# Optimization experiments

Measured on AMD Instinct MI355X. Metric: run time of the kernel, lower is better.

Reference implementation:

```python
import jax, jax.numpy as jnp
import numpy as np

N = 3072        # nodes
F_IN = 512      # input_dim
F_OUT = 256     # output_dim
ORDER = 2       # Cayley polynomial order
JACOBI = 3      # Jacobi fixed-point iterations per order


def setup_inputs() -> dict:
    key = jax.random.key(0)
    k1, k2, k3, k4, k5 = jax.random.split(key, 5)
    # normalized-adjacency-like matrix: row sums ~1 so h*Laplacian is well scaled
    adj = jax.random.uniform(k1, (N, N), dtype=jnp.float32) * (2.0 / N)
    x = jax.random.normal(k2, (N, F_IN), dtype=jnp.float32)
    h = jnp.float32(1.0)  # spectral zoom parameter
    w0 = jax.random.normal(k3, (F_IN, F_OUT), dtype=jnp.float32) * 0.05
    wr = jax.random.normal(k4, (ORDER, F_IN, F_OUT), dtype=jnp.float32) * 0.05
    wi = jax.random.normal(k5, (ORDER, F_IN, F_OUT), dtype=jnp.float32) * 0.05
    return {"x": x, "adj": adj, "h": h, "w0": w0, "wr": wr, "wi": wi}


def _cayley_forward(x, adj, h, w0, wr, wi):
    c64 = jnp.complex64
    j1 = jnp.asarray(1j, dtype=c64)
    n = adj.shape[0]
    I = jnp.eye(n, dtype=jnp.float32)
    # h * Laplacian, L = I - A_norm  (complex64, as in the TF code)
    hL = (h * (I - adj)).astype(c64)
    # Jacobi diagonal: rowsum(hL) + i  (constant across iterations)
    diag_inv = 1.0 / (jnp.sum(hL, axis=1) + j1)  # [n]

    # support[0] = I  ->  real part of I @ (x @ w0) is just x @ w0
    out = x @ w0  # [n, F_OUT] float32

    xc = x.astype(c64)
    csum = jnp.zeros((n, w0.shape[1]), dtype=c64)
    prev = I.astype(c64)
    for j in range(ORDER):
        # rhs of the linear system: x_j = hL @ prev - i*prev
        xj = hL @ prev - j1 * prev
        # Jacobi iterations: y <- y + D^{-1} (x_j - (hL @ y + i*y))
        y = xj
        for _ in range(JACOBI):
            y = y + diag_inv[:, None] * (xj - (hL @ y + j1 * y))
        W = jax.lax.complex(wr[j], wi[j])          # [F_IN, F_OUT] complex64
        csum = csum + y @ (xc @ W)                  # support_j @ pre_sup
        prev = y
    out = out + 2.0 * jnp.real(csum).astype(jnp.float32)
    return jax.nn.relu(out)


def reference(x, adj, h, w0, wr, wi):
    return _cayley_forward(x, adj, h, w0, wr, wi)
```

## Files before the change

kernel.cpp:

```cpp
#include <hip/hip_runtime.h>
#include <hip/hip_bf16.h>

#define NN 3072
#define FIN 512
#define FOUT 256

typedef __attribute__((ext_vector_type(8))) short short8;
typedef __attribute__((ext_vector_type(4))) float f32x4;

__device__ __forceinline__ short f2bf(float f) {
  union { float f; unsigned u; } v; v.f = f;
  unsigned r = v.u + 0x7fffu + ((v.u >> 16) & 1u);
  return (short)(r >> 16);
}

__device__ __forceinline__ void glds16(const short* g, short* l) {
  __builtin_amdgcn_global_load_lds(
      (const __attribute__((address_space(1))) unsigned*)g,
      (__attribute__((address_space(3))) unsigned*)l, 16, 0, 0);
}

template<int N> __device__ __forceinline__ void wait_vm() {
  if constexpr (N == 0)      asm volatile("s_waitcnt vmcnt(0)" ::: "memory");
  else if constexpr (N == 6) asm volatile("s_waitcnt vmcnt(6)" ::: "memory");
  else                       asm volatile("s_waitcnt vmcnt(8)" ::: "memory");
}


__global__ __launch_bounds__(256) void prep_adj(const float* __restrict__ adj,
    short* __restrict__ adjbf, float2* __restrict__ dinv, const float* __restrict__ hptr)
{
  int m = blockIdx.x;
  int tid = threadIdx.x;
  const float4* row = (const float4*)(adj + (size_t)m * NN);
  short4* obf = (short4*)(adjbf + (size_t)m * NN);
  float sum = 0.f;
#pragma unroll
  for (int i = 0; i < NN / 4 / 256; ++i) {
    int idx = i * 256 + tid;
    float4 v = row[idx];
    sum += (v.x + v.y) + (v.z + v.w);
    obf[idx] = make_short4(f2bf(v.x), f2bf(v.y), f2bf(v.z), f2bf(v.w));
  }
#pragma unroll
  for (int off = 32; off > 0; off >>= 1) sum += __shfl_down(sum, off, 64);
  __shared__ float red[4];
  if ((tid & 63) == 0) red[tid >> 6] = sum;
  __syncthreads();
  if (tid == 0) {
    float s = red[0] + red[1] + red[2] + red[3];
    float h = hptr[0];
    float r = h * (1.f - s);
    float den = r * r + 1.f;
    dinv[m] = make_float2(r / den, -1.f / den);
  }
}

__global__ __launch_bounds__(256) void prep_x(const float* __restrict__ x, short* __restrict__ xbf) {
  int idx = blockIdx.x * 256 + threadIdx.x;
  float4 v = ((const float4*)x)[idx];
  ((short4*)xbf)[idx] = make_short4(f2bf(v.x), f2bf(v.y), f2bf(v.z), f2bf(v.w));
}

__global__ __launch_bounds__(256) void prep_w(const float* __restrict__ w0,
    const float* __restrict__ wr, const float* __restrict__ wi, short* __restrict__ wpack)
{
  int idx = blockIdx.x * 256 + threadIdx.x;
  int f = idx & 511;
  int i = idx >> 9;
  float v;
  if (i < 1024) {
    int j = (i < 512) ? 1 : 0;
    int local = i & 511;
    int c = local >> 1;
    const float* src = (local & 1) ? wi : wr;
    v = src[((size_t)j * FIN + f) * FOUT + c];
  } else {
    v = w0[(size_t)f * FOUT + (i - 1024)];
  }
  wpack[idx] = f2bf(v);
}

template<int BM, int MR, int MODE, int KTOT>
__global__ __launch_bounds__(512, 2) void gemm_k(
    const short* __restrict__ Apan, int lda,
    const short* __restrict__ Badj, int ldb,
    const float* __restrict__ Vin,
    const float* __restrict__ Yin,
    float* __restrict__ Fout,
    short* __restrict__ Bout,
    const float2* __restrict__ dinv,
    const float* __restrict__ hptr)
{
  constexpr int BK = 64;
  constexpr int NT = KTOT / (2 * BK);
  constexpr int ALOADS = BM / 8;
  constexpr int BLOADS = 16;
  constexpr int LPW = (ALOADS + BLOADS) / 4;

  __shared__ short As[2][2][BM * BK];
  __shared__ short Bs[2][2][128 * BK];

  const int tid  = threadIdx.x;
  const int lane = tid & 63;
  const int w    = tid >> 6;
  const int g    = w >> 2;
  const int wg   = w & 3;
  const int wrow = wg >> 1, wcol = wg & 1;
  const int l15  = lane & 15;

  const int i0 = blockIdx.y * BM;
  const int j0 = blockIdx.x * 128;
  const int kbase = g * (KTOT / 2);

  const int srow = lane >> 3;
  const int scol = ((lane & 7) ^ srow) * 8;

  const short* aSrc = Apan + (size_t)i0 * lda + kbase;
  const short* bSrc = Badj + (size_t)j0 * ldb + kbase;

  auto STAGE = [&](int t) {
    const int k0 = t * BK;
    short* at = As[g][t & 1];
    short* bt = Bs[g][t & 1];
#pragma unroll
    for (int li = 0; li < ALOADS / 4; ++li) {
      int rb = (wg + li * 4) * 8;
      glds16(aSrc + (size_t)(rb + srow) * lda + k0 + scol, at + rb * BK);
    }
#pragma unroll
    for (int li = 0; li < BLOADS / 4; ++li) {
      int rb = (wg + li * 4) * 8;
      glds16(bSrc + (size_t)(rb + srow) * ldb + k0 + scol, bt + rb * BK);
    }
  };

  f32x4 acc[MR][4];
#pragma unroll
  for (int a = 0; a < MR; a++)
#pragma unroll
    for (int b = 0; b < 4; b++) acc[a][b] = (f32x4){0.f, 0.f, 0.f, 0.f};

  STAGE(0);
  STAGE(1);

  for (int t = 0; t < NT; ++t) {
    if (t < NT - 1) wait_vm<LPW>(); else wait_vm<0>();
    __builtin_amdgcn_s_barrier();
    asm volatile("" ::: "memory");

    const short* at = As[g][t & 1];
    const short* bt = Bs[g][t & 1];
#pragma unroll
    for (int kk = 0; kk < 2; ++kk) {
      const int cbase = kk * 4 + (lane >> 4);
      short8 af[MR], bfg[4];
#pragma unroll
      for (int a = 0; a < MR; ++a) {
        int ra = wrow * (MR * 16) + a * 16 + l15;
        int c = cbase ^ (ra & 7);
        af[a] = *(const short8*)(at + ra * BK + c * 8);
      }
#pragma unroll
      for (int b = 0; b < 4; ++b) {
        int rb = wcol * 64 + b * 16 + l15;
        int c = cbase ^ (rb & 7);
        bfg[b] = *(const short8*)(bt + rb * BK + c * 8);
      }
      __builtin_amdgcn_s_setprio(1);
#pragma unroll
      for (int a = 0; a < MR; ++a)
#pragma unroll
        for (int b = 0; b < 4; ++b)
          acc[a][b] = __builtin_amdgcn_mfma_f32_16x16x32_bf16(af[a], bfg[b], acc[a][b], 0, 0, 0);
      __builtin_amdgcn_s_setprio(0);
    }

    asm volatile("" ::: "memory");
    __builtin_amdgcn_s_barrier();
    asm volatile("" ::: "memory");
    if (t + 2 < NT) STAGE(t + 2);
  }

  float* red = (float*)&As[0][0][0];
  const int rl0 = wrow * (MR * 16) + ((lane >> 4) << 2);
  const int cl0 = wcol * 64 + l15;
  if (g == 1) {
#pragma unroll
    for (int a = 0; a < MR; ++a)
#pragma unroll
      for (int b = 0; b < 4; ++b)
#pragma unroll
        for (int q = 0; q < 4; ++q)
          red[(size_t)(rl0 + a * 16 + q) * 128 + cl0 + b * 16] = acc[a][b][q];
  }
  __syncthreads();

  if (g == 0) {
    const float hv = hptr[0];
#pragma unroll
    for (int a = 0; a < MR; ++a) {
#pragma unroll
      for (int b = 0; b < 4; ++b) {
        f32x4 c = acc[a][b];
        const int rl = rl0 + a * 16;
        const int cl = cl0 + b * 16;
#pragma unroll
        for (int q = 0; q < 4; ++q)
          c[q] += red[(size_t)(rl + q) * 128 + cl];
        const int ia = i0 + rl;
        const int jb = j0 + cl;
        if (MODE == 0) {
#pragma unroll
          for (int q = 0; q < 4; ++q) {
            size_t off = (size_t)(ia + q) * NN + jb;
            Fout[off] = c[q];
            if (ia + q < 1024) Bout[off] = f2bf(c[q]);
          }
        } else if (MODE == 1) {
#pragma unroll
          for (int p = 0; p < 4; p += 2) {
            size_t offr = (size_t)(ia + p) * NN + jb;
            size_t offi = offr + NN;
            float vr = Vin[offr], vi = Vin[offi];
            float outr = hv * (vr - c[p])     + vi;
            float outi = hv * (vi - c[p + 1]) - vr;
            Fout[offr] = outr; Fout[offi] = outi;
            Bout[offr] = f2bf(outr); Bout[offi] = f2bf(outi);
          }
        } else {
#pragma unroll
          for (int p = 0; p < 4; p += 2) {
            size_t offr = (size_t)(ia + p) * NN + jb;
            size_t offi = offr + NN;
            float2 dv = dinv[jb];
            float vr = Vin[offr], vi = Vin[offi];
            float yr = Yin[offr], yi = Yin[offi];
            float tr_ = hv * (yr - c[p])     - yi;
            float ti_ = hv * (yi - c[p + 1]) + yr;
            float er = vr - tr_, ei = vi - ti_;
            float nyr = yr + dv.x * er - dv.y * ei;
            float nyi = yi + dv.x * ei + dv.y * er;
            Fout[offr] = nyr; Fout[offi] = nyi;
            Bout[offr] = f2bf(nyr); Bout[offi] = f2bf(nyi);
          }
        }
      }
    }
  }
}

__global__ __launch_bounds__(256) void final_out(
    const float* __restrict__ Vbuf,
    const float* __restrict__ ybuf,
    float* __restrict__ out)
{
  __shared__ float t[64][65];
  int n0 = blockIdx.x * 64;
  int c0 = blockIdx.y * 64;
  int lane = threadIdx.x & 63;
  int wv = threadIdx.x >> 6;
#pragma unroll
  for (int s = 0; s < 16; s++) {
    int c = c0 + wv + s * 4;
    float o0 = Vbuf[(size_t)(1024 + c) * NN + n0 + lane];
    float u  = ybuf[(size_t)(2 * c) * NN + n0 + lane];
    float sv = ybuf[(size_t)(512 + 2 * c) * NN + n0 + lane];
    float v = o0 + 2.f * (u + sv);
    t[lane][wv + s * 4] = v > 0.f ? v : 0.f;
  }
  __syncthreads();
#pragma unroll
  for (int s = 0; s < 16; s++) {
    int nl = wv + s * 4;
    out[(size_t)(n0 + nl) * FOUT + c0 + lane] = t[nl][lane];
  }
}

extern "C" void kernel_launch(void* const* d_in, const int* in_sizes, int n_in,
                              void* d_out, int out_size, void* d_ws, size_t ws_size,
                              hipStream_t stream) {
  const float* x   = (const float*)d_in[0];
  const float* adj = (const float*)d_in[1];
  const float* h   = (const float*)d_in[2];
  const float* w0  = (const float*)d_in[3];
  const float* wr  = (const float*)d_in[4];
  const float* wi  = (const float*)d_in[5];
  float* out = (float*)d_out;

  char* ws = (char*)d_ws;
  size_t off = 0;
  auto alloc = [&](size_t bytes) {
    char* p = ws + off;
    off += (bytes + 255) & ~(size_t)255;
    return p;
  };
  short*  adjbf = (short*)alloc((size_t)NN * NN * 2);
  short*  xbf   = (short*)alloc((size_t)NN * FIN * 2);
  short*  wpack = (short*)alloc((size_t)1280 * FIN * 2);
  float2* dinv  = (float2*)alloc((size_t)NN * sizeof(float2));
  float*  Vbuf  = (float*)alloc((size_t)1280 * NN * 4);
  float*  ybuf  = (float*)alloc((size_t)1024 * NN * 4);
  short*  b0    = (short*)alloc((size_t)1024 * NN * 2);
  short*  b1    = (short*)alloc((size_t)1024 * NN * 2);

  prep_adj<<<NN, 256, 0, stream>>>(adj, adjbf, dinv, h);
  prep_x<<<(NN * FIN / 4) / 256, 256, 0, stream>>>(x, xbf);
  prep_w<<<(1280 * FIN) / 256, 256, 0, stream>>>(w0, wr, wi, wpack);

  gemm_k<128, 4, 0, FIN><<<dim3(24, 10), 512, 0, stream>>>(
      wpack, FIN, xbf, FIN, nullptr, nullptr, Vbuf, b0, dinv, h);
  gemm_k<128, 4, 1, NN><<<dim3(24, 8), 512, 0, stream>>>(
      b0, NN, adjbf, NN, Vbuf, nullptr, Vbuf, b1, dinv, h);
  gemm_k<128, 4, 2, NN><<<dim3(24, 8), 512, 0, stream>>>(
      b1, NN, adjbf, NN, Vbuf, Vbuf, ybuf, b0, dinv, h);
  gemm_k<128, 4, 2, NN><<<dim3(24, 8), 512, 0, stream>>>(
      b0, NN, adjbf, NN, Vbuf, ybuf, ybuf, b1, dinv, h);
  gemm_k<128, 4, 2, NN><<<dim3(24, 8), 512, 0, stream>>>(
      b1, NN, adjbf, NN, Vbuf, ybuf, ybuf, b0, dinv, h);
  gemm_k<64, 2, 1, NN><<<dim3(24, 8), 512, 0, stream>>>(
      b0, NN, adjbf, NN, ybuf, nullptr, Vbuf, b1, dinv, h);
  gemm_k<64, 2, 2, NN><<<dim3(24, 8), 512, 0, stream>>>(
      b1, NN, adjbf, NN, Vbuf, Vbuf, ybuf, b0, dinv, h);
  gemm_k<64, 2, 2, NN><<<dim3(24, 8), 512, 0, stream>>>(
      b0, NN, adjbf, NN, Vbuf, ybuf, ybuf, b1, dinv, h);
  gemm_k<64, 2, 2, NN><<<dim3(24, 8), 512, 0, stream>>>(
      b1, NN, adjbf, NN, Vbuf, ybuf, ybuf, b0, dinv, h);

  final_out<<<dim3(48, 4), 256, 0, stream>>>(Vbuf, ybuf, out);
}
```

Baseline: 387.6 us.

## Replace intra-block split-K GEMM with cross-block split-K and atomic tile reduction

The two-group in-block K split with double-buffered LDS is replaced by a single-group 256-thread kernel. It splits K across up to 4 blocks, each writing fp32 partials to a workspace slab. The last block to arrive, detected with a per-tile atomic counter, reduces the partials and runs the fused epilogue. Block indices are remapped so column tiles group by XCD. This raises the number of blocks per GEMM to fill the CUs, but drops double buffering, adds fp32 partial traffic and needs a counter memset.

```diff
diff --git a/kernel.cpp b/kernel.cpp
--- a/kernel.cpp
+++ b/kernel.cpp
@@ -18,12 +18,6 @@
   __builtin_amdgcn_global_load_lds(
       (const __attribute__((address_space(1))) unsigned*)g,
       (__attribute__((address_space(3))) unsigned*)l, 16, 0, 0);
-}
-
-template<int N> __device__ __forceinline__ void wait_vm() {
-  if constexpr (N == 0)      asm volatile("s_waitcnt vmcnt(0)" ::: "memory");
-  else if constexpr (N == 6) asm volatile("s_waitcnt vmcnt(6)" ::: "memory");
-  else                       asm volatile("s_waitcnt vmcnt(8)" ::: "memory");
 }
 
 
@@ -81,37 +75,44 @@
   wpack[idx] = f2bf(v);
 }
 
-template<int BM, int MR, int MODE, int KTOT>
-__global__ __launch_bounds__(512, 2) void gemm_k(
+__global__ __launch_bounds__(256, 4) void gemm_sk(
     const short* __restrict__ Apan, int lda,
     const short* __restrict__ Badj, int ldb,
+    int rows, int sk, int kper, int mode,
     const float* __restrict__ Vin,
     const float* __restrict__ Yin,
     float* __restrict__ Fout,
     short* __restrict__ Bout,
+    float* __restrict__ partial,
+    int* __restrict__ cnt,
     const float2* __restrict__ dinv,
     const float* __restrict__ hptr)
 {
   constexpr int BK = 64;
-  constexpr int NT = KTOT / (2 * BK);
-  constexpr int ALOADS = BM / 8;
-  constexpr int BLOADS = 16;
-  constexpr int LPW = (ALOADS + BLOADS) / 4;
-
-  __shared__ short As[2][2][BM * BK];
-  __shared__ short Bs[2][2][128 * BK];
+  const size_t SLAB = (size_t)1280 * NN;
+
+  __shared__ short As[128 * BK];
+  __shared__ short Bs[128 * BK];
+  __shared__ int s_ord;
 
   const int tid  = threadIdx.x;
   const int lane = tid & 63;
   const int w    = tid >> 6;
-  const int g    = w >> 2;
-  const int wg   = w & 3;
-  const int wrow = wg >> 1, wcol = wg & 1;
   const int l15  = lane & 15;
 
-  const int i0 = blockIdx.y * BM;
-  const int j0 = blockIdx.x * 128;
-  const int kbase = g * (KTOT / 2);
+  const int f    = blockIdx.x;
+  const int xcd  = f & 7;
+  const int s    = f >> 3;
+  const int perj = rows * sk;
+  const int j    = xcd * 3 + s / perj;
+  const int rr   = s % perj;
+  const int i    = rr % rows;
+  const int z    = rr / rows;
+
+  const int i0 = i * 128;
+  const int j0 = j * 128;
+  const int kbase = z * kper;
+  const int NT = kper / BK;
 
   const int srow = lane >> 3;
   const int scol = ((lane & 7) ^ srow) * 8;
@@ -121,129 +122,125 @@
 
   auto STAGE = [&](int t) {
     const int k0 = t * BK;
-    short* at = As[g][t & 1];
-    short* bt = Bs[g][t & 1];
-#pragma unroll
-    for (int li = 0; li < ALOADS / 4; ++li) {
-      int rb = (wg + li * 4) * 8;
-      glds16(aSrc + (size_t)(rb + srow) * lda + k0 + scol, at + rb * BK);
-    }
-#pragma unroll
-    for (int li = 0; li < BLOADS / 4; ++li) {
-      int rb = (wg + li * 4) * 8;
-      glds16(bSrc + (size_t)(rb + srow) * ldb + k0 + scol, bt + rb * BK);
+#pragma unroll
+    for (int li = 0; li < 4; ++li) {
+      int rb = (w + li * 4) * 8;
+      glds16(aSrc + (size_t)(rb + srow) * lda + k0 + scol, As + rb * BK);
+      glds16(bSrc + (size_t)(rb + srow) * ldb + k0 + scol, Bs + rb * BK);
     }
   };
 
-  f32x4 acc[MR][4];
-#pragma unroll
-  for (int a = 0; a < MR; a++)
+  f32x4 acc[4][4];
+#pragma unroll
+  for (int a = 0; a < 4; a++)
 #pragma unroll
     for (int b = 0; b < 4; b++) acc[a][b] = (f32x4){0.f, 0.f, 0.f, 0.f};
 
+  const int wrow = w >> 1, wcol = w & 1;
+
   STAGE(0);
-  STAGE(1);
-
   for (int t = 0; t < NT; ++t) {
-    if (t < NT - 1) wait_vm<LPW>(); else wait_vm<0>();
-    __builtin_amdgcn_s_barrier();
-    asm volatile("" ::: "memory");
-
-    const short* at = As[g][t & 1];
-    const short* bt = Bs[g][t & 1];
+    __syncthreads();
 #pragma unroll
     for (int kk = 0; kk < 2; ++kk) {
-      const int cbase = kk * 4 + (lane >> 4);
-      short8 af[MR], bfg[4];
-#pragma unroll
-      for (int a = 0; a < MR; ++a) {
-        int ra = wrow * (MR * 16) + a * 16 + l15;
-        int c = cbase ^ (ra & 7);
-        af[a] = *(const short8*)(at + ra * BK + c * 8);
+      const int cb = kk * 4 + (lane >> 4);
+      short8 af[4], bfr[4];
+#pragma unroll
+      for (int a = 0; a < 4; ++a) {
+        int ra = wrow * 64 + a * 16 + l15;
+        int c = cb ^ (ra & 7);
+        af[a] = *(const short8*)(As + ra * BK + c * 8);
       }
 #pragma unroll
       for (int b = 0; b < 4; ++b) {
         int rb = wcol * 64 + b * 16 + l15;
-        int c = cbase ^ (rb & 7);
-        bfg[b] = *(const short8*)(bt + rb * BK + c * 8);
-      }
-      __builtin_amdgcn_s_setprio(1);
-#pragma unroll
-      for (int a = 0; a < MR; ++a)
+        int c = cb ^ (rb & 7);
+        bfr[b] = *(const short8*)(Bs + rb * BK + c * 8);
+      }
+#pragma unroll
+      for (int a = 0; a < 4; ++a)
 #pragma unroll
         for (int b = 0; b < 4; ++b)
-          acc[a][b] = __builtin_amdgcn_mfma_f32_16x16x32_bf16(af[a], bfg[b], acc[a][b], 0, 0, 0);
-      __builtin_amdgcn_s_setprio(0);
+          acc[a][b] = __builtin_amdgcn_mfma_f32_16x16x32_bf16(af[a], bfr[b], acc[a][b], 0, 0, 0);
     }
-
-    asm volatile("" ::: "memory");
-    __builtin_amdgcn_s_barrier();
-    asm volatile("" ::: "memory");
-    if (t + 2 < NT) STAGE(t + 2);
-  }
-
-  float* red = (float*)&As[0][0][0];
-  const int rl0 = wrow * (MR * 16) + ((lane >> 4) << 2);
-  const int cl0 = wcol * 64 + l15;
-  if (g == 1) {
-#pragma unroll
-    for (int a = 0; a < MR; ++a)
-#pragma unroll
-      for (int b = 0; b < 4; ++b)
+    __syncthreads();
+    if (t + 1 < NT) STAGE(t + 1);
+  }
+
+  const int ib = i0 + wrow * 64 + ((lane >> 4) << 2);
+  const int tile = j * rows + i;
+
+  if (sk > 1) {
+    float* ps = partial + (size_t)z * SLAB;
+#pragma unroll
+    for (int a = 0; a < 4; ++a) {
+      int ia = ib + a * 16;
+#pragma unroll
+      for (int b = 0; b < 4; ++b) {
+        int jb = j0 + wcol * 64 + b * 16 + l15;
 #pragma unroll
         for (int q = 0; q < 4; ++q)
-          red[(size_t)(rl0 + a * 16 + q) * 128 + cl0 + b * 16] = acc[a][b][q];
-  }
-  __syncthreads();
-
-  if (g == 0) {
-    const float hv = hptr[0];
-#pragma unroll
-    for (int a = 0; a < MR; ++a) {
-#pragma unroll
-      for (int b = 0; b < 4; ++b) {
-        f32x4 c = acc[a][b];
-        const int rl = rl0 + a * 16;
-        const int cl = cl0 + b * 16;
-#pragma unroll
-        for (int q = 0; q < 4; ++q)
-          c[q] += red[(size_t)(rl + q) * 128 + cl];
-        const int ia = i0 + rl;
-        const int jb = j0 + cl;
-        if (MODE == 0) {
-#pragma unroll
-          for (int q = 0; q < 4; ++q) {
-            size_t off = (size_t)(ia + q) * NN + jb;
-            Fout[off] = c[q];
-            if (ia + q < 1024) Bout[off] = f2bf(c[q]);
-          }
-        } else if (MODE == 1) {
-#pragma unroll
-          for (int p = 0; p < 4; p += 2) {
-            size_t offr = (size_t)(ia + p) * NN + jb;
-            size_t offi = offr + NN;
-            float vr = Vin[offr], vi = Vin[offi];
-            float outr = hv * (vr - c[p])     + vi;
-            float outi = hv * (vi - c[p + 1]) - vr;
-            Fout[offr] = outr; Fout[offi] = outi;
-            Bout[offr] = f2bf(outr); Bout[offi] = f2bf(outi);
-          }
-        } else {
-#pragma unroll
-          for (int p = 0; p < 4; p += 2) {
-            size_t offr = (size_t)(ia + p) * NN + jb;
-            size_t offi = offr + NN;
-            float2 dv = dinv[jb];
-            float vr = Vin[offr], vi = Vin[offi];
-            float yr = Yin[offr], yi = Yin[offi];
-            float tr_ = hv * (yr - c[p])     - yi;
-            float ti_ = hv * (yi - c[p + 1]) + yr;
-            float er = vr - tr_, ei = vi - ti_;
-            float nyr = yr + dv.x * er - dv.y * ei;
-            float nyi = yi + dv.x * ei + dv.y * er;
-            Fout[offr] = nyr; Fout[offi] = nyi;
-            Bout[offr] = f2bf(nyr); Bout[offi] = f2bf(nyi);
-          }
+          ps[(size_t)(ia + q) * NN + jb] = acc[a][b][q];
+      }
+    }
+    __threadfence();
+    __syncthreads();
+    if (tid == 0) s_ord = atomicAdd(&cnt[tile], 1);
+    __syncthreads();
+    if (s_ord != sk - 1) return;
+    __threadfence();
+  }
+
+  const float hv = hptr[0];
+#pragma unroll
+  for (int a = 0; a < 4; ++a) {
+    int ia = ib + a * 16;
+#pragma unroll
+    for (int b = 0; b < 4; ++b) {
+      int jb = j0 + wcol * 64 + b * 16 + l15;
+      f32x4 c = acc[a][b];
+      if (sk > 1) {
+        for (int z2 = 0; z2 < sk; ++z2) {
+          if (z2 == z) continue;
+          const float* ps = partial + (size_t)z2 * SLAB;
+#pragma unroll
+          for (int q = 0; q < 4; ++q)
+            c[q] += ps[(size_t)(ia + q) * NN + jb];
+        }
+      }
+      if (mode == 0) {
+#pragma unroll
+        for (int q = 0; q < 4; ++q) {
+          size_t off = (size_t)(ia + q) * NN + jb;
+          Fout[off] = c[q];
+          if (ia + q < 1024) Bout[off] = f2bf(c[q]);
+        }
+      } else if (mode == 1) {
+#pragma unroll
+        for (int p = 0; p < 4; p += 2) {
+          size_t offr = (size_t)(ia + p) * NN + jb;
+          size_t offi = offr + NN;
+          float vr = Vin[offr], vi = Vin[offi];
+          float outr = hv * (vr - c[p])     + vi;
+          float outi = hv * (vi - c[p + 1]) - vr;
+          Fout[offr] = outr; Fout[offi] = outi;
+          Bout[offr] = f2bf(outr); Bout[offi] = f2bf(outi);
+        }
+      } else {
+#pragma unroll
+        for (int p = 0; p < 4; p += 2) {
+          size_t offr = (size_t)(ia + p) * NN + jb;
+          size_t offi = offr + NN;
+          float2 dv = dinv[jb];
+          float vr = Vin[offr], vi = Vin[offi];
+          float yr = Yin[offr], yi = Yin[offi];
+          float tr_ = hv * (yr - c[p])     - yi;
+          float ti_ = hv * (yi - c[p + 1]) + yr;
+          float er = vr - tr_, ei = vi - ti_;
+          float nyr = yr + dv.x * er - dv.y * ei;
+          float nyi = yi + dv.x * ei + dv.y * er;
+          Fout[offr] = nyr; Fout[offi] = nyi;
+          Bout[offr] = f2bf(nyr); Bout[offi] = f2bf(nyi);
         }
       }
     }
@@ -304,28 +301,37 @@
   short*  b0    = (short*)alloc((size_t)1024 * NN * 2);
   short*  b1    = (short*)alloc((size_t)1024 * NN * 2);
 
+  size_t slab = (size_t)1280 * NN * 4;
+  size_t cntB = 9 * 256 * sizeof(int);
+  int sk = 1;
+  if (ws_size >= off + 4 * slab + cntB + 4096) sk = 4;
+  else if (ws_size >= off + 2 * slab + cntB + 4096) sk = 2;
+  float* partial = (float*)alloc((size_t)sk * slab);
+  int*   cnt     = (int*)alloc(cntB);
+  int sk0 = (sk >= 2) ? 2 : 1;
+
+  hipMemsetAsync(cnt, 0, cntB, stream);
   prep_adj<<<NN, 256, 0, stream>>>(adj, adjbf, dinv, h);
   prep_x<<<(NN * FIN / 4) / 256, 256, 0, stream>>>(x, xbf);
   prep_w<<<(1280 * FIN) / 256, 256, 0, stream>>>(w0, wr, wi, wpack);
 
-  gemm_k<128, 4, 0, FIN><<<dim3(24, 10), 512, 0, stream>>>(
-      wpack, FIN, xbf, FIN, nullptr, nullptr, Vbuf, b0, dinv, h);
-  gemm_k<128, 4, 1, NN><<<dim3(24, 8), 512, 0, stream>>>(
-      b0, NN, adjbf, NN, Vbuf, nullptr, Vbuf, b1, dinv, h);
-  gemm_k<128, 4, 2, NN><<<dim3(24, 8), 512, 0, stream>>>(
-      b1, NN, adjbf, NN, Vbuf, Vbuf, ybuf, b0, dinv, h);
-  gemm_k<128, 4, 2, NN><<<dim3(24, 8), 512, 0, stream>>>(
-      b0, NN, adjbf, NN, Vbuf, ybuf, ybuf, b1, dinv, h);
-  gemm_k<128, 4, 2, NN><<<dim3(24, 8), 512, 0, stream>>>(
-      b1, NN, adjbf, NN, Vbuf, ybuf, ybuf, b0, dinv, h);
-  gemm_k<64, 2, 1, NN><<<dim3(24, 8), 512, 0, stream>>>(
-      b0, NN, adjbf, NN, ybuf, nullptr, Vbuf, b1, dinv, h);
-  gemm_k<64, 2, 2, NN><<<dim3(24, 8), 512, 0, stream>>>(
-      b1, NN, adjbf, NN, Vbuf, Vbuf, ybuf, b0, dinv, h);
-  gemm_k<64, 2, 2, NN><<<dim3(24, 8), 512, 0, stream>>>(
-      b0, NN, adjbf, NN, Vbuf, ybuf, ybuf, b1, dinv, h);
-  gemm_k<64, 2, 2, NN><<<dim3(24, 8), 512, 0, stream>>>(
-      b1, NN, adjbf, NN, Vbuf, ybuf, ybuf, b0, dinv, h);
+  auto G = [&](int rows, int skv, int kper, int mode,
+               const short* A, int lda, const short* B, int ldb,
+               const float* Vin, const float* Yin, float* Fout, short* Bout, int didx) {
+    gemm_sk<<<dim3(24 * rows * skv), 256, 0, stream>>>(
+        A, lda, B, ldb, rows, skv, kper, mode,
+        Vin, Yin, Fout, Bout, partial, cnt + didx * 256, dinv, h);
+  };
+
+  G(10, sk0, FIN / sk0, 0, wpack, FIN, xbf, FIN, nullptr, nullptr, Vbuf, b0, 0);
+  G(8, sk, NN / sk, 1, b0, NN, adjbf, NN, Vbuf, nullptr, Vbuf, b1, 1);
+  G(8, sk, NN / sk, 2, b1, NN, adjbf, NN, Vbuf, Vbuf, ybuf, b0, 2);
+  G(8, sk, NN / sk, 2, b0, NN, adjbf, NN, Vbuf, ybuf, ybuf, b1, 3);
+  G(8, sk, NN / sk, 2, b1, NN, adjbf, NN, Vbuf, ybuf, ybuf, b0, 4);
+  G(4, sk, NN / sk, 1, b0, NN, adjbf, NN, ybuf, nullptr, Vbuf, b1, 5);
+  G(4, sk, NN / sk, 2, b1, NN, adjbf, NN, Vbuf, Vbuf, ybuf, b0, 6);
+  G(4, sk, NN / sk, 2, b0, NN, adjbf, NN, Vbuf, ybuf, ybuf, b1, 7);
+  G(4, sk, NN / sk, 2, b1, NN, adjbf, NN, Vbuf, ybuf, ybuf, b0, 8);
 
   final_out<<<dim3(48, 4), 256, 0, stream>>>(Vbuf, ybuf, out);
 }
```

After: 1.375 ms. 255% more time.

## Replace split-K 512-thread GEMM with 64x96 tiles and no reduction

Applied to the files above, without the earlier changes.

Replaces the split-K GEMM, where two 4-wave groups each handled half of K and were reduced through LDS, with a single 4-wave block that runs the full K loop over a 64x96 output tile. The grid grows from 24x8 to 32x16 (or 32x8) blocks, so more CUs get work on the 256-CU part and the LDS reduction and extra sync go away. In exchange each block does twice as many K iterations, has smaller MFMA tiles with less operand reuse, and drops the setprio hints.

```diff
diff --git a/kernel.cpp b/kernel.cpp
--- a/kernel.cpp
+++ b/kernel.cpp
@@ -22,8 +22,8 @@
 
 template<int N> __device__ __forceinline__ void wait_vm() {
   if constexpr (N == 0)      asm volatile("s_waitcnt vmcnt(0)" ::: "memory");
-  else if constexpr (N == 6) asm volatile("s_waitcnt vmcnt(6)" ::: "memory");
-  else                       asm volatile("s_waitcnt vmcnt(8)" ::: "memory");
+  else if constexpr (N == 5) asm volatile("s_waitcnt vmcnt(5)" ::: "memory");
+  else                       asm volatile("s_waitcnt vmcnt(10)" ::: "memory");
 }
 
 
@@ -81,8 +81,8 @@
   wpack[idx] = f2bf(v);
 }
 
-template<int BM, int MR, int MODE, int KTOT>
-__global__ __launch_bounds__(512, 2) void gemm_k(
+template<int MODE, int KTOT>
+__global__ __launch_bounds__(256, 2) void gemm_t(
     const short* __restrict__ Apan, int lda,
     const short* __restrict__ Badj, int ldb,
     const float* __restrict__ Vin,
@@ -93,53 +93,53 @@
     const float* __restrict__ hptr)
 {
   constexpr int BK = 64;
-  constexpr int NT = KTOT / (2 * BK);
-  constexpr int ALOADS = BM / 8;
-  constexpr int BLOADS = 16;
-  constexpr int LPW = (ALOADS + BLOADS) / 4;
-
-  __shared__ short As[2][2][BM * BK];
-  __shared__ short Bs[2][2][128 * BK];
+  constexpr int BM = 64;
+  constexpr int BN = 96;
+  constexpr int NT = KTOT / BK;
+  constexpr int MR = 2;
+  constexpr int AL = 2;
+  constexpr int BL = 3;
+  constexpr int LPW = AL + BL;
+
+  __shared__ short As[2][BM * BK];
+  __shared__ short Bs[2][BN * BK];
 
   const int tid  = threadIdx.x;
   const int lane = tid & 63;
   const int w    = tid >> 6;
-  const int g    = w >> 2;
-  const int wg   = w & 3;
-  const int wrow = wg >> 1, wcol = wg & 1;
   const int l15  = lane & 15;
+  const int wrow = w >> 1, wcol = w & 1;
 
   const int i0 = blockIdx.y * BM;
-  const int j0 = blockIdx.x * 128;
-  const int kbase = g * (KTOT / 2);
+  const int j0 = blockIdx.x * BN;
 
   const int srow = lane >> 3;
   const int scol = ((lane & 7) ^ srow) * 8;
 
-  const short* aSrc = Apan + (size_t)i0 * lda + kbase;
-  const short* bSrc = Badj + (size_t)j0 * ldb + kbase;
+  const short* aSrc = Apan + (size_t)i0 * lda;
+  const short* bSrc = Badj + (size_t)j0 * ldb;
 
   auto STAGE = [&](int t) {
     const int k0 = t * BK;
-    short* at = As[g][t & 1];
-    short* bt = Bs[g][t & 1];
-#pragma unroll
-    for (int li = 0; li < ALOADS / 4; ++li) {
-      int rb = (wg + li * 4) * 8;
+    short* at = As[t & 1];
+    short* bt = Bs[t & 1];
+#pragma unroll
+    for (int li = 0; li < AL; ++li) {
+      int rb = (w + li * 4) * 8;
       glds16(aSrc + (size_t)(rb + srow) * lda + k0 + scol, at + rb * BK);
     }
 #pragma unroll
-    for (int li = 0; li < BLOADS / 4; ++li) {
-      int rb = (wg + li * 4) * 8;
+    for (int li = 0; li < BL; ++li) {
+      int rb = (w + li * 4) * 8;
       glds16(bSrc + (size_t)(rb + srow) * ldb + k0 + scol, bt + rb * BK);
     }
   };
 
-  f32x4 acc[MR][4];
+  f32x4 acc[MR][3];
 #pragma unroll
   for (int a = 0; a < MR; a++)
 #pragma unroll
-    for (int b = 0; b < 4; b++) acc[a][b] = (f32x4){0.f, 0.f, 0.f, 0.f};
+    for (int b = 0; b < 3; b++) acc[a][b] = (f32x4){0.f, 0.f, 0.f, 0.f};
 
   STAGE(0);
   STAGE(1);
@@ -149,31 +149,29 @@
     __builtin_amdgcn_s_barrier();
     asm volatile("" ::: "memory");
 
-    const short* at = As[g][t & 1];
-    const short* bt = Bs[g][t & 1];
+    const short* at = As[t & 1];
+    const short* bt = Bs[t & 1];
 #pragma unroll
     for (int kk = 0; kk < 2; ++kk) {
-      const int cbase = kk * 4 + (lane >> 4);
-      short8 af[MR], bfg[4];
+      const int cb = kk * 4 + (lane >> 4);
+      short8 af[MR], bfr[3];
 #pragma unroll
       for (int a = 0; a < MR; ++a) {
-        int ra = wrow * (MR * 16) + a * 16 + l15;
-        int c = cbase ^ (ra & 7);
+        int ra = wrow * 32 + a * 16 + l15;
+        int c = cb ^ (ra & 7);
         af[a] = *(const short8*)(at + ra * BK + c * 8);
       }
 #pragma unroll
-      for (int b = 0; b < 4; ++b) {
-        int rb = wcol * 64 + b * 16 + l15;
-        int c = cbase ^ (rb & 7);
-        bfg[b] = *(const short8*)(bt + rb * BK + c * 8);
+      for (int b = 0; b < 3; ++b) {
+        int rb = wcol * 48 + b * 16 + l15;
+        int c = cb ^ (rb & 7);
+        bfr[b] = *(const short8*)(bt + rb * BK + c * 8);
       }
-      __builtin_amdgcn_s_setprio(1);
 #pragma unroll
       for (int a = 0; a < MR; ++a)
 #pragma unroll
-        for (int b = 0; b < 4; ++b)
-          acc[a][b] = __builtin_amdgcn_mfma_f32_16x16x32_bf16(af[a], bfg[b], acc[a][b], 0, 0, 0);
-      __builtin_amdgcn_s_setprio(0);
+        for (int b = 0; b < 3; ++b)
+          acc[a][b] = __builtin_amdgcn_mfma_f32_16x16x32_bf16(af[a], bfr[b], acc[a][b], 0, 0, 0);
     }
 
     asm volatile("" ::: "memory");
@@ -182,68 +180,48 @@
     if (t + 2 < NT) STAGE(t + 2);
   }
 
-  float* red = (float*)&As[0][0][0];
-  const int rl0 = wrow * (MR * 16) + ((lane >> 4) << 2);
-  const int cl0 = wcol * 64 + l15;
-  if (g == 1) {
-#pragma unroll
-    for (int a = 0; a < MR; ++a)
-#pragma unroll
-      for (int b = 0; b < 4; ++b)
-#pragma unroll
-        for (int q = 0; q < 4; ++q)
-          red[(size_t)(rl0 + a * 16 + q) * 128 + cl0 + b * 16] = acc[a][b][q];
-  }
-  __syncthreads();
-
-  if (g == 0) {
-    const float hv = hptr[0];
-#pragma unroll
-    for (int a = 0; a < MR; ++a) {
-#pragma unroll
-      for (int b = 0; b < 4; ++b) {
-        f32x4 c = acc[a][b];
-        const int rl = rl0 + a * 16;
-        const int cl = cl0 + b * 16;
-#pragma unroll
-        for (int q = 0; q < 4; ++q)
-          c[q] += red[(size_t)(rl + q) * 128 + cl];
-        const int ia = i0 + rl;
-        const int jb = j0 + cl;
-        if (MODE == 0) {
-#pragma unroll
-          for (int q = 0; q < 4; ++q) {
-            size_t off = (size_t)(ia + q) * NN + jb;
-            Fout[off] = c[q];
-            if (ia + q < 1024) Bout[off] = f2bf(c[q]);
-          }
-        } else if (MODE == 1) {
-#pragma unroll
-          for (int p = 0; p < 4; p += 2) {
-            size_t offr = (size_t)(ia + p) * NN + jb;
-            size_t offi = offr + NN;
-            float vr = Vin[offr], vi = Vin[offi];
-            float outr = hv * (vr - c[p])     + vi;
-            float outi = hv * (vi - c[p + 1]) - vr;
-            Fout[offr] = outr; Fout[offi] = outi;
-            Bout[offr] = f2bf(outr); Bout[offi] = f2bf(outi);
-          }
-        } else {
-#pragma unroll
-          for (int p = 0; p < 4; p += 2) {
-            size_t offr = (size_t)(ia + p) * NN + jb;
-            size_t offi = offr + NN;
-            float2 dv = dinv[jb];
-            float vr = Vin[offr], vi = Vin[offi];
-            float yr = Yin[offr], yi = Yin[offi];
-            float tr_ = hv * (yr - c[p])     - yi;
-            float ti_ = hv * (yi - c[p + 1]) + yr;
-            float er = vr - tr_, ei = vi - ti_;
-            float nyr = yr + dv.x * er - dv.y * ei;
-            float nyi = yi + dv.x * ei + dv.y * er;
-            Fout[offr] = nyr; Fout[offi] = nyi;
-            Bout[offr] = f2bf(nyr); Bout[offi] = f2bf(nyi);
-          }
+  const float hv = hptr[0];
+  const int ibase = i0 + wrow * 32 + ((lane >> 4) << 2);
+#pragma unroll
+  for (int a = 0; a < MR; ++a) {
+    const int ia = ibase + a * 16;
+#pragma unroll
+    for (int b = 0; b < 3; ++b) {
+      const int jb = j0 + wcol * 48 + b * 16 + l15;
+      f32x4 c = acc[a][b];
+      if (MODE == 0) {
+#pragma unroll
+        for (int q = 0; q < 4; ++q) {
+          size_t off = (size_t)(ia + q) * NN + jb;
+          Fout[off] = c[q];
+          if (ia + q < 1024) Bout[off] = f2bf(c[q]);
+        }
+      } else if (MODE == 1) {
+#pragma unroll
+        for (int p = 0; p < 4; p += 2) {
+          size_t offr = (size_t)(ia + p) * NN + jb;
+          size_t offi = offr + NN;
+          float vr = Vin[offr], vi = Vin[offi];
+          float outr = hv * (vr - c[p])     + vi;
+          float outi = hv * (vi - c[p + 1]) - vr;
+          Fout[offr] = outr; Fout[offi] = outi;
+          Bout[offr] = f2bf(outr); Bout[offi] = f2bf(outi);
+        }
+      } else {
+#pragma unroll
+        for (int p = 0; p < 4; p += 2) {
+          size_t offr = (size_t)(ia + p) * NN + jb;
+          size_t offi = offr + NN;
+          float2 dv = dinv[jb];
+          float vr = Vin[offr], vi = Vin[offi];
+          float yr = Yin[offr], yi = Yin[offi];
+          float tr_ = hv * (yr - c[p])     - yi;
+          float ti_ = hv * (yi - c[p + 1]) + yr;
+          float er = vr - tr_, ei = vi - ti_;
+          float nyr = yr + dv.x * er - dv.y * ei;
+          float nyi = yi + dv.x * ei + dv.y * er;
+          Fout[offr] = nyr; Fout[offi] = nyi;
+          Bout[offr] = f2bf(nyr); Bout[offi] = f2bf(nyi);
         }
       }
     }
@@ -308,23 +286,23 @@
   prep_x<<<(NN * FIN / 4) / 256, 256, 0, stream>>>(x, xbf);
   prep_w<<<(1280 * FIN) / 256, 256, 0, stream>>>(w0, wr, wi, wpack);
 
-  gemm_k<128, 4, 0, FIN><<<dim3(24, 10), 512, 0, stream>>>(
+  gemm_t<0, FIN><<<dim3(32, 20), 256, 0, stream>>>(
       wpack, FIN, xbf, FIN, nullptr, nullptr, Vbuf, b0, dinv, h);
-  gemm_k<128, 4, 1, NN><<<dim3(24, 8), 512, 0, stream>>>(
+  gemm_t<1, NN><<<dim3(32, 16), 256, 0, stream>>>(
       b0, NN, adjbf, NN, Vbuf, nullptr, Vbuf, b1, dinv, h);
-  gemm_k<128, 4, 2, NN><<<dim3(24, 8), 512, 0, stream>>>(
+  gemm_t<2, NN><<<dim3(32, 16), 256, 0, stream>>>(
       b1, NN, adjbf, NN, Vbuf, Vbuf, ybuf, b0, dinv, h);
-  gemm_k<128, 4, 2, NN><<<dim3(24, 8), 512, 0, stream>>>(
+  gemm_t<2, NN><<<dim3(32, 16), 256, 0, stream>>>(
       b0, NN, adjbf, NN, Vbuf, ybuf, ybuf, b1, dinv, h);
-  gemm_k<128, 4, 2, NN><<<dim3(24, 8), 512, 0, stream>>>(
+  gemm_t<2, NN><<<dim3(32, 16), 256, 0, stream>>>(
       b1, NN, adjbf, NN, Vbuf, ybuf, ybuf, b0, dinv, h);
-  gemm_k<64, 2, 1, NN><<<dim3(24, 8), 512, 0, stream>>>(
+  gemm_t<1, NN><<<dim3(32, 8), 256, 0, stream>>>(
       b0, NN, adjbf, NN, ybuf, nullptr, Vbuf, b1, dinv, h);
-  gemm_k<64, 2, 2, NN><<<dim3(24, 8), 512, 0, stream>>>(
+  gemm_t<2, NN><<<dim3(32, 8), 256, 0, stream>>>(
       b1, NN, adjbf, NN, Vbuf, Vbuf, ybuf, b0, dinv, h);
-  gemm_k<64, 2, 2, NN><<<dim3(24, 8), 512, 0, stream>>>(
+  gemm_t<2, NN><<<dim3(32, 8), 256, 0, stream>>>(
       b0, NN, adjbf, NN, Vbuf, ybuf, ybuf, b1, dinv, h);
-  gemm_k<64, 2, 2, NN><<<dim3(24, 8), 512, 0, stream>>>(
+  gemm_t<2, NN><<<dim3(32, 8), 256, 0, stream>>>(
       b1, NN, adjbf, NN, Vbuf, ybuf, ybuf, b0, dinv, h);
 
   final_out<<<dim3(48, 4), 256, 0, stream>>>(Vbuf, ybuf, out);
```

Measured after the change: 376.2 us. 2.9% less time.

## Use 96-wide N tiles with XCD-aware block mapping and merge prep kernels

Applied to the files above, without the earlier changes.

Shrinks the GEMM N tile from 128 to 96 columns, which grows the grid from 192 to 256 blocks to fill the MI355X's 256 CUs. It also replaces the 2D grid with a 1D index that keeps each XCD on a contiguous group of column tiles, aiming for better L2 reuse of the adjacency panel. The x and weight conversion kernels are merged into one launch. The smaller tile lowers per-block compute intensity, and the LDS load counts and waitcnt values had to be retuned to match.

```diff
diff --git a/kernel.cpp b/kernel.cpp
--- a/kernel.cpp
+++ b/kernel.cpp
@@ -22,8 +22,8 @@
 
 template<int N> __device__ __forceinline__ void wait_vm() {
   if constexpr (N == 0)      asm volatile("s_waitcnt vmcnt(0)" ::: "memory");
-  else if constexpr (N == 6) asm volatile("s_waitcnt vmcnt(6)" ::: "memory");
-  else                       asm volatile("s_waitcnt vmcnt(8)" ::: "memory");
+  else if constexpr (N == 5) asm volatile("s_waitcnt vmcnt(5)" ::: "memory");
+  else                       asm volatile("s_waitcnt vmcnt(7)" ::: "memory");
 }
 
 
@@ -56,35 +56,38 @@
   }
 }
 
-__global__ __launch_bounds__(256) void prep_x(const float* __restrict__ x, short* __restrict__ xbf) {
-  int idx = blockIdx.x * 256 + threadIdx.x;
-  float4 v = ((const float4*)x)[idx];
-  ((short4*)xbf)[idx] = make_short4(f2bf(v.x), f2bf(v.y), f2bf(v.z), f2bf(v.w));
-}
-
-__global__ __launch_bounds__(256) void prep_w(const float* __restrict__ w0,
-    const float* __restrict__ wr, const float* __restrict__ wi, short* __restrict__ wpack)
+__global__ __launch_bounds__(256) void prep_xw(const float* __restrict__ x,
+    const float* __restrict__ w0, const float* __restrict__ wr,
+    const float* __restrict__ wi, short* __restrict__ xbf, short* __restrict__ wpack)
 {
-  int idx = blockIdx.x * 256 + threadIdx.x;
-  int f = idx & 511;
-  int i = idx >> 9;
-  float v;
-  if (i < 1024) {
-    int j = (i < 512) ? 1 : 0;
-    int local = i & 511;
-    int c = local >> 1;
-    const float* src = (local & 1) ? wi : wr;
-    v = src[((size_t)j * FIN + f) * FOUT + c];
+  int b = blockIdx.x;
+  if (b < 1536) {
+    int idx = b * 256 + threadIdx.x;
+    float4 v = ((const float4*)x)[idx];
+    ((short4*)xbf)[idx] = make_short4(f2bf(v.x), f2bf(v.y), f2bf(v.z), f2bf(v.w));
   } else {
-    v = w0[(size_t)f * FOUT + (i - 1024)];
-  }
-  wpack[idx] = f2bf(v);
-}
-
-template<int BM, int MR, int MODE, int KTOT>
-__global__ __launch_bounds__(512, 2) void gemm_k(
+    int idx = (b - 1536) * 256 + threadIdx.x;
+    int f = idx & 511;
+    int i = idx >> 9;
+    float v;
+    if (i < 1024) {
+      int j = (i < 512) ? 1 : 0;
+      int local = i & 511;
+      int c = local >> 1;
+      const float* src = (local & 1) ? wi : wr;
+      v = src[((size_t)j * FIN + f) * FOUT + c];
+    } else {
+      v = w0[(size_t)f * FOUT + (i - 1024)];
+    }
+    wpack[idx] = f2bf(v);
+  }
+}
+
+template<int BM, int MODE, int KTOT>
+__global__ __launch_bounds__(512, 2) void gemm_g(
     const short* __restrict__ Apan, int lda,
     const short* __restrict__ Badj, int ldb,
+    int itiles,
     const float* __restrict__ Vin,
     const float* __restrict__ Yin,
     float* __restrict__ Fout,
@@ -93,53 +96,57 @@
     const float* __restrict__ hptr)
 {
   constexpr int BK = 64;
-  constexpr int NT = KTOT / (2 * BK);
-  constexpr int ALOADS = BM / 8;
-  constexpr int BLOADS = 16;
-  constexpr int LPW = (ALOADS + BLOADS) / 4;
+  constexpr int BN = 96;
+  constexpr int NT = KTOT / 2 / BK;
+  constexpr int MR = BM / 32;
+  constexpr int LPW = MR + 3;
 
   __shared__ short As[2][2][BM * BK];
-  __shared__ short Bs[2][2][128 * BK];
+  __shared__ short Bs[2][2][BN * BK];
 
   const int tid  = threadIdx.x;
   const int lane = tid & 63;
   const int w    = tid >> 6;
   const int g    = w >> 2;
   const int wg   = w & 3;
+  const int l15  = lane & 15;
   const int wrow = wg >> 1, wcol = wg & 1;
-  const int l15  = lane & 15;
-
-  const int i0 = blockIdx.y * BM;
-  const int j0 = blockIdx.x * 128;
-  const int kbase = g * (KTOT / 2);
+
+  const int bid = blockIdx.x;
+  const int xcd = bid & 7;
+  const int s   = bid >> 3;
+  const int jt  = xcd * 4 + s / itiles;
+  const int it  = s % itiles;
+  const int i0  = it * BM;
+  const int j0  = jt * BN;
 
   const int srow = lane >> 3;
   const int scol = ((lane & 7) ^ srow) * 8;
 
-  const short* aSrc = Apan + (size_t)i0 * lda + kbase;
-  const short* bSrc = Badj + (size_t)j0 * ldb + kbase;
+  const short* aSrc = Apan + (size_t)i0 * lda + g * (KTOT / 2);
+  const short* bSrc = Badj + (size_t)j0 * ldb + g * (KTOT / 2);
 
   auto STAGE = [&](int t) {
     const int k0 = t * BK;
     short* at = As[g][t & 1];
     short* bt = Bs[g][t & 1];
 #pragma unroll
-    for (int li = 0; li < ALOADS / 4; ++li) {
+    for (int li = 0; li < MR; ++li) {
       int rb = (wg + li * 4) * 8;
       glds16(aSrc + (size_t)(rb + srow) * lda + k0 + scol, at + rb * BK);
     }
 #pragma unroll
-    for (int li = 0; li < BLOADS / 4; ++li) {
+    for (int li = 0; li < 3; ++li) {
       int rb = (wg + li * 4) * 8;
       glds16(bSrc + (size_t)(rb + srow) * ldb + k0 + scol, bt + rb * BK);
     }
   };
 
-  f32x4 acc[MR][4];
+  f32x4 acc[MR][3];
 #pragma unroll
   for (int a = 0; a < MR; a++)
 #pragma unroll
-    for (int b = 0; b < 4; b++) acc[a][b] = (f32x4){0.f, 0.f, 0.f, 0.f};
+    for (int b = 0; b < 3; b++) acc[a][b] = (f32x4){0.f, 0.f, 0.f, 0.f};
 
   STAGE(0);
   STAGE(1);
@@ -153,26 +160,26 @@
     const short* bt = Bs[g][t & 1];
 #pragma unroll
     for (int kk = 0; kk < 2; ++kk) {
-      const int cbase = kk * 4 + (lane >> 4);
-      short8 af[MR], bfg[4];
+      const int cb = kk * 4 + (lane >> 4);
+      short8 af[MR], bfr[3];
 #pragma unroll
       for (int a = 0; a < MR; ++a) {
-        int ra = wrow * (MR * 16) + a * 16 + l15;
-        int c = cbase ^ (ra & 7);
+        int ra = wrow * (BM / 2) + a * 16 + l15;
+        int c = cb ^ (ra & 7);
         af[a] = *(const short8*)(at + ra * BK + c * 8);
       }
 #pragma unroll
-      for (int b = 0; b < 4; ++b) {
-        int rb = wcol * 64 + b * 16 + l15;
-        int c = cbase ^ (rb & 7);
-        bfg[b] = *(const short8*)(bt + rb * BK + c * 8);
+      for (int b = 0; b < 3; ++b) {
+        int rb = wcol * 48 + b * 16 + l15;
+        int c = cb ^ (rb & 7);
+        bfr[b] = *(const short8*)(bt + rb * BK + c * 8);
       }
       __builtin_amdgcn_s_setprio(1);
 #pragma unroll
       for (int a = 0; a < MR; ++a)
 #pragma unroll
-        for (int b = 0; b < 4; ++b)
-          acc[a][b] = __builtin_amdgcn_mfma_f32_16x16x32_bf16(af[a], bfg[b], acc[a][b], 0, 0, 0);
+        for (int b = 0; b < 3; ++b)
+          acc[a][b] = __builtin_amdgcn_mfma_f32_16x16x32_bf16(af[a], bfr[b], acc[a][b], 0, 0, 0);
       __builtin_amdgcn_s_setprio(0);
     }
 
@@ -183,67 +190,66 @@
   }
 
   float* red = (float*)&As[0][0][0];
-  const int rl0 = wrow * (MR * 16) + ((lane >> 4) << 2);
-  const int cl0 = wcol * 64 + l15;
+  const int rl0 = wrow * (BM / 2) + ((lane >> 4) << 2);
+  const int cl0 = wcol * 48 + l15;
   if (g == 1) {
 #pragma unroll
     for (int a = 0; a < MR; ++a)
 #pragma unroll
-      for (int b = 0; b < 4; ++b)
+      for (int b = 0; b < 3; ++b)
 #pragma unroll
         for (int q = 0; q < 4; ++q)
-          red[(size_t)(rl0 + a * 16 + q) * 128 + cl0 + b * 16] = acc[a][b][q];
+          red[(size_t)(rl0 + a * 16 + q) * BN + cl0 + b * 16] = acc[a][b][q];
   }
   __syncthreads();
-
-  if (g == 0) {
-    const float hv = hptr[0];
-#pragma unroll
-    for (int a = 0; a < MR; ++a) {
-#pragma unroll
-      for (int b = 0; b < 4; ++b) {
-        f32x4 c = acc[a][b];
-        const int rl = rl0 + a * 16;
-        const int cl = cl0 + b * 16;
-#pragma unroll
-        for (int q = 0; q < 4; ++q)
-          c[q] += red[(size_t)(rl + q) * 128 + cl];
-        const int ia = i0 + rl;
-        const int jb = j0 + cl;
-        if (MODE == 0) {
-#pragma unroll
-          for (int q = 0; q < 4; ++q) {
-            size_t off = (size_t)(ia + q) * NN + jb;
-            Fout[off] = c[q];
-            if (ia + q < 1024) Bout[off] = f2bf(c[q]);
-          }
-        } else if (MODE == 1) {
-#pragma unroll
-          for (int p = 0; p < 4; p += 2) {
-            size_t offr = (size_t)(ia + p) * NN + jb;
-            size_t offi = offr + NN;
-            float vr = Vin[offr], vi = Vin[offi];
-            float outr = hv * (vr - c[p])     + vi;
-            float outi = hv * (vi - c[p + 1]) - vr;
-            Fout[offr] = outr; Fout[offi] = outi;
-            Bout[offr] = f2bf(outr); Bout[offi] = f2bf(outi);
-          }
-        } else {
-#pragma unroll
-          for (int p = 0; p < 4; p += 2) {
-            size_t offr = (size_t)(ia + p) * NN + jb;
-            size_t offi = offr + NN;
-            float2 dv = dinv[jb];
-            float vr = Vin[offr], vi = Vin[offi];
-            float yr = Yin[offr], yi = Yin[offi];
-            float tr_ = hv * (yr - c[p])     - yi;
-            float ti_ = hv * (yi - c[p + 1]) + yr;
-            float er = vr - tr_, ei = vi - ti_;
-            float nyr = yr + dv.x * er - dv.y * ei;
-            float nyi = yi + dv.x * ei + dv.y * er;
-            Fout[offr] = nyr; Fout[offi] = nyi;
-            Bout[offr] = f2bf(nyr); Bout[offi] = f2bf(nyi);
-          }
+  if (g == 1) return;
+
+  const float hv = hptr[0];
+#pragma unroll
+  for (int a = 0; a < MR; ++a) {
+    const int rl = rl0 + a * 16;
+    const int ia = i0 + rl;
+#pragma unroll
+    for (int b = 0; b < 3; ++b) {
+      const int cl = cl0 + b * 16;
+      const int jb = j0 + cl;
+      f32x4 c = acc[a][b];
+#pragma unroll
+      for (int q = 0; q < 4; ++q)
+        c[q] += red[(size_t)(rl + q) * BN + cl];
+      if (MODE == 0) {
+#pragma unroll
+        for (int q = 0; q < 4; ++q) {
+          size_t off = (size_t)(ia + q) * NN + jb;
+          Fout[off] = c[q];
+          if (ia + q < 1024) Bout[off] = f2bf(c[q]);
+        }
+      } else if (MODE == 1) {
+#pragma unroll
+        for (int p = 0; p < 4; p += 2) {
+          size_t offr = (size_t)(ia + p) * NN + jb;
+          size_t offi = offr + NN;
+          float vr = Vin[offr], vi = Vin[offi];
+          float outr = hv * (vr - c[p])     + vi;
+          float outi = hv * (vi - c[p + 1]) - vr;
+          Fout[offr] = outr; Fout[offi] = outi;
+          Bout[offr] = f2bf(outr); Bout[offi] = f2bf(outi);
+        }
+      } else {
+#pragma unroll
+        for (int p = 0; p < 4; p += 2) {
+          size_t offr = (size_t)(ia + p) * NN + jb;
+          size_t offi = offr + NN;
+          float2 dv = dinv[jb];
+          float vr = Vin[offr], vi = Vin[offi];
+          float yr = Yin[offr], yi = Yin[offi];
+          float tr_ = hv * (yr - c[p])     - yi;
+          float ti_ = hv * (yi - c[p + 1]) + yr;
+          float er = vr - tr_, ei = vi - ti_;
+          float nyr = yr + dv.x * er - dv.y * ei;
+          float nyi = yi + dv.x * ei + dv.y * er;
+          Fout[offr] = nyr; Fout[offi] = nyi;
+          Bout[offr] = f2bf(nyr); Bout[offi] = f2bf(nyi);
         }
       }
     }
@@ -305,27 +311,26 @@
   short*  b1    = (short*)alloc((size_t)1024 * NN * 2);
 
   prep_adj<<<NN, 256, 0, stream>>>(adj, adjbf, dinv, h);
-  prep_x<<<(NN * FIN / 4) / 256, 256, 0, stream>>>(x, xbf);
-  prep_w<<<(1280 * FIN) / 256, 256, 0, stream>>>(w0, wr, wi, wpack);
-
-  gemm_k<128, 4, 0, FIN><<<dim3(24, 10), 512, 0, stream>>>(
-      wpack, FIN, xbf, FIN, nullptr, nullptr, Vbuf, b0, dinv, h);
-  gemm_k<128, 4, 1, NN><<<dim3(24, 8), 512, 0, stream>>>(
-      b0, NN, adjbf, NN, Vbuf, nullptr, Vbuf, b1, dinv, h);
-  gemm_k<128, 4, 2, NN><<<dim3(24, 8), 512, 0, stream>>>(
-      b1, NN, adjbf, NN, Vbuf, Vbuf, ybuf, b0, dinv, h);
-  gemm_k<128, 4, 2, NN><<<dim3(24, 8), 512, 0, stream>>>(
-      b0, NN, adjbf, NN, Vbuf, ybuf, ybuf, b1, dinv, h);
-  gemm_k<128, 4, 2, NN><<<dim3(24, 8), 512, 0, stream>>>(
-      b1, NN, adjbf, NN, Vbuf, ybuf, ybuf, b0, dinv, h);
-  gemm_k<64, 2, 1, NN><<<dim3(24, 8), 512, 0, stream>>>(
-      b0, NN, adjbf, NN, ybuf, nullptr, Vbuf, b1, dinv, h);
-  gemm_k<64, 2, 2, NN><<<dim3(24, 8), 512, 0, stream>>>(
-      b1, NN, adjbf, NN, Vbuf, Vbuf, ybuf, b0, dinv, h);
-  gemm_k<64, 2, 2, NN><<<dim3(24, 8), 512, 0, stream>>>(
-      b0, NN, adjbf, NN, Vbuf, ybuf, ybuf, b1, dinv, h);
-  gemm_k<64, 2, 2, NN><<<dim3(24, 8), 512, 0, stream>>>(
-      b1, NN, adjbf, NN, Vbuf, ybuf, ybuf, b0, dinv, h);
+  prep_xw<<<4096, 256, 0, stream>>>(x, w0, wr, wi, xbf, wpack);
+
+  gemm_g<128, 0, FIN><<<dim3(32 * 10), 512, 0, stream>>>(
+      wpack, FIN, xbf, FIN, 10, nullptr, nullptr, Vbuf, b0, dinv, h);
+  gemm_g<128, 1, NN><<<dim3(32 * 8), 512, 0, stream>>>(
+      b0, NN, adjbf, NN, 8, Vbuf, nullptr, Vbuf, b1, dinv, h);
+  gemm_g<128, 2, NN><<<dim3(32 * 8), 512, 0, stream>>>(
+      b1, NN, adjbf, NN, 8, Vbuf, Vbuf, ybuf, b0, dinv, h);
+  gemm_g<128, 2, NN><<<dim3(32 * 8), 512, 0, stream>>>(
+      b0, NN, adjbf, NN, 8, Vbuf, ybuf, ybuf, b1, dinv, h);
+  gemm_g<128, 2, NN><<<dim3(32 * 8), 512, 0, stream>>>(
+      b1, NN, adjbf, NN, 8, Vbuf, ybuf, ybuf, b0, dinv, h);
+  gemm_g<64, 1, NN><<<dim3(32 * 8), 512, 0, stream>>>(
+      b0, NN, adjbf, NN, 8, ybuf, nullptr, Vbuf, b1, dinv, h);
+  gemm_g<64, 2, NN><<<dim3(32 * 8), 512, 0, stream>>>(
+      b1, NN, adjbf, NN, 8, Vbuf, Vbuf, ybuf, b0, dinv, h);
+  gemm_g<64, 2, NN><<<dim3(32 * 8), 512, 0, stream>>>(
+      b0, NN, adjbf, NN, 8, Vbuf, ybuf, ybuf, b1, dinv, h);
+  gemm_g<64, 2, NN><<<dim3(32 * 8), 512, 0, stream>>>(
+      b1, NN, adjbf, NN, 8, Vbuf, ybuf, ybuf, b0, dinv, h);
 
   final_out<<<dim3(48, 4), 256, 0, stream>>>(Vbuf, ybuf, out);
 }
```

Measured after the change: 362.0 us. 1.07x faster.
